# Kernel optimization log

Measured on AMD Instinct MI355X. Metric: run time of the kernel, lower is better.

Reference implementation:

```python
import jax, jax.numpy as jnp
import numpy as np

NUM_HEADS = 32
HEAD_DIM = 128
NUM_KV_HEADS = 8
SCALE = 0.08838834764831845  # 1/sqrt(128)
T = 2048          # total packed tokens (total_q == total_k in delta branch)
N_SAL = 512       # number of salient rows
NUM_SEQS = 4
EPS = 1e-8
NEG = -1e30


def setup_inputs() -> dict:
    key = jax.random.key(0)
    ks = jax.random.split(key, 5)
    q = jax.random.normal(ks[0], (T, NUM_HEADS, HEAD_DIM), dtype=jnp.float32)
    k = jax.random.normal(ks[1], (T, NUM_KV_HEADS, HEAD_DIM), dtype=jnp.float32)
    v = jax.random.normal(ks[2], (N_SAL, NUM_KV_HEADS, HEAD_DIM), dtype=jnp.float32)
    v_cache = jax.random.normal(ks[3], (T, NUM_KV_HEADS, HEAD_DIM), dtype=jnp.float32)
    c_cache = jax.random.normal(ks[4], (T, NUM_HEADS * HEAD_DIM), dtype=jnp.float32)
    # unique, sorted salient row indices (torch index_copy requires well-defined scatter)
    idx_salient_row = (jnp.arange(N_SAL, dtype=jnp.int64) * (T // N_SAL))
    # 4 equal packed sequences
    cu_seqlens = jnp.array([0, 512, 1024, 1536, 2048], dtype=jnp.int64)
    return {"q": q, "k": k, "v": v, "v_cache": v_cache, "c_cache": c_cache,
            "idx_salient_row": idx_salient_row, "cu_seqlens": cu_seqlens}


def _segment_ids(cu_seqlens, n):
    # seg[i] = which packed sequence row i belongs to (searchsorted right on bounds)
    return jnp.searchsorted(cu_seqlens[1:], jnp.arange(n), side="right")


def _sdpa(q_, k_, v_, seg_q_, seg_k_):
    # GQA: repeat_interleave kv heads to match query heads
    n_rep = q_.shape[1] // k_.shape[1]
    if n_rep > 1:
        k_ = jnp.repeat(k_, n_rep, axis=1)
        v_ = jnp.repeat(v_, n_rep, axis=1)
    scores = jnp.einsum("qhd,khd->hqk", q_, k_) * SCALE  # [H, nq, T]
    allow = (seg_q_[:, None] == seg_k_[None, :])          # [nq, T]
    scores = jnp.where(allow[None, :, :], scores, NEG)
    p = jax.nn.softmax(scores, axis=-1)
    return jnp.einsum("hqk,khd->qhd", p, v_)              # [nq, H, D]


def reference(q, k, v, v_cache, c_cache, idx_salient_row, cu_seqlens):
    total = q.shape[0]
    seg = _segment_ids(cu_seqlens, total)  # seg_q == seg_k (total_q == total_k)

    # delta KV-cache update at salient rows
    v_delta = v - v_cache[idx_salient_row]                      # [n_sal, Hkv, D]
    v_delta_sparse = jnp.zeros_like(k).at[idx_salient_row].set(v_delta)
    v_cache_new = v_cache.at[idx_salient_row].set(v)

    # salient-row full attention against updated cache
    o_salient = _sdpa(q[idx_salient_row], k, v_cache_new, seg[idx_salient_row], seg)
    # sparse delta attention for every row
    delta_c = _sdpa(q, k, v_delta_sparse, seg, seg)

    new_c_flat = c_cache + delta_c.reshape(total, -1)
    new_c_flat = new_c_flat.at[idx_salient_row].set(o_salient.reshape(o_salient.shape[0], -1))

    # cosine similarity between old and new context (early-exit signal)
    num = jnp.sum(c_cache * new_c_flat, axis=-1)
    den_c = jnp.sum(c_cache * c_cache, axis=-1)
    den_n = jnp.sum(new_c_flat * new_c_flat, axis=-1)
    cos_sim = num / (jnp.sqrt(den_c) * jnp.sqrt(den_n) + EPS)

    return new_c_flat.reshape(total, NUM_HEADS, HEAD_DIM), cos_sim
```

## Files before the change

### kernel.cpp

```cpp
#include <hip/hip_runtime.h>
#include <math.h>

#define NUM_HEADS 32
#define HEAD_DIM 128
#define NUM_KV_HEADS 8
#define SCALE 0.08838834764831845f
#define EPS 1e-8f
#define MAX_SEG 512
#define QT 32
#define BLK 512
#define SEGC_MAX 16
#define PD_CHUNKS 4
#define SAL_PAD 576
#define PB_STRIDE 520
#define PD_STRIDE 136
#define TLD 130
#define CD (NUM_HEADS * HEAD_DIM)

typedef __bf16 bf16x8 __attribute__((ext_vector_type(8)));
typedef __bf16 bf16x4 __attribute__((ext_vector_type(4)));
typedef float  f32x4  __attribute__((ext_vector_type(4)));

__device__ __forceinline__ int lower_bound_i(const int* __restrict__ a, int n, int key) {
    int lo = 0, hi = n;
    while (lo < hi) { int mid = (lo + hi) >> 1; if (a[mid] < key) lo = mid + 1; else hi = mid; }
    return lo;
}
__device__ __forceinline__ int bsearch_eq(const int* __restrict__ a, int n, int key) {
    int lo = lower_bound_i(a, n, key);
    return (lo < n && a[lo] == key) ? lo : -1;
}

__global__ void prep(const float* __restrict__ k, const float* __restrict__ v,
                     const float* __restrict__ vc, const int* __restrict__ idx,
                     __bf16* __restrict__ kb, __bf16* __restrict__ vnewT,
                     __bf16* __restrict__ vdT, int T, int Tpad, int n_sal,
                     int nb_conv, int nb_vt) {
    __shared__ __bf16 tile[64 * TLD];
    __shared__ int sal_of[64];
    const int b = blockIdx.x;
    const int tid = threadIdx.x;

    if (b < nb_conv) {
        int i = b * 256 + tid;
        int n8 = T * NUM_KV_HEADS * HEAD_DIM / 8;
        if (i < n8) {
            const float4* s4 = (const float4*)(k + (size_t)i * 8);
            float4 a = s4[0], bb = s4[1];
            bf16x8 o;
            o[0]=(__bf16)a.x; o[1]=(__bf16)a.y; o[2]=(__bf16)a.z; o[3]=(__bf16)a.w;
            o[4]=(__bf16)bb.x; o[5]=(__bf16)bb.y; o[6]=(__bf16)bb.z; o[7]=(__bf16)bb.w;
            *(bf16x8*)(kb + (size_t)i * 8) = o;
        }
        return;
    }
    if (b < nb_conv + nb_vt * NUM_KV_HEADS) {
        const int bb = b - nb_conv;
        const int kv = bb / nb_vt;
        const int r0 = (bb % nb_vt) * 64;
        if (tid < 64) sal_of[tid] = bsearch_eq(idx, n_sal, r0 + tid);
        __syncthreads();
        for (int ii = tid; ii < 64 * 32; ii += 256) {
            int r = ii >> 5, c4 = ii & 31;
            int row = r0 + r;
            float4 f = {0.f, 0.f, 0.f, 0.f};
            if (row < T) {
                int s2 = sal_of[r];
                const float* src = (s2 >= 0)
                    ? v  + ((size_t)s2  * NUM_KV_HEADS + kv) * HEAD_DIM
                    : vc + ((size_t)row * NUM_KV_HEADS + kv) * HEAD_DIM;
                f = *(const float4*)(src + c4 * 4);
            }
            __bf16* tp = &tile[r * TLD + c4 * 4];
            tp[0] = (__bf16)f.x; tp[1] = (__bf16)f.y; tp[2] = (__bf16)f.z; tp[3] = (__bf16)f.w;
        }
        __syncthreads();
        for (int ii = tid; ii < 128 * 8; ii += 256) {
            int d = ii >> 3, rg = ii & 7;
            int row_out = r0 + rg * 8;
            if (row_out < Tpad) {
                bf16x8 o;
#pragma unroll
                for (int j = 0; j < 8; j++) o[j] = tile[(rg * 8 + j) * TLD + d];
                *(bf16x8*)(vnewT + ((size_t)kv * HEAD_DIM + d) * Tpad + row_out) = o;
            }
        }
        return;
    }
    {
        const int bb = b - nb_conv - nb_vt * NUM_KV_HEADS;
        const int nvd = SAL_PAD / 64;
        const int kv = bb / nvd;
        const int s0 = (bb % nvd) * 64;
        for (int ii = tid; ii < 64 * 32; ii += 256) {
            int r = ii >> 5, c4 = ii & 31;
            int s = s0 + r;
            float4 f = {0.f, 0.f, 0.f, 0.f};
            if (s < n_sal) {
                int row = idx[s];
                float4 a = *(const float4*)(v  + ((size_t)s   * NUM_KV_HEADS + kv) * HEAD_DIM + c4 * 4);
                float4 bb2 = *(const float4*)(vc + ((size_t)row * NUM_KV_HEADS + kv) * HEAD_DIM + c4 * 4);
                f.x = a.x - bb2.x; f.y = a.y - bb2.y; f.z = a.z - bb2.z; f.w = a.w - bb2.w;
            }
            __bf16* tp = &tile[r * TLD + c4 * 4];
            tp[0] = (__bf16)f.x; tp[1] = (__bf16)f.y; tp[2] = (__bf16)f.z; tp[3] = (__bf16)f.w;
        }
        __syncthreads();
        for (int ii = tid; ii < 128 * 8; ii += 256) {
            int d = ii >> 3, rg = ii & 7;
            bf16x8 o;
#pragma unroll
            for (int j = 0; j < 8; j++) o[j] = tile[(rg * 8 + j) * TLD + d];
            *(bf16x8*)(vdT + ((size_t)kv * HEAD_DIM + d) * SAL_PAD + s0 + rg * 8) = o;
        }
    }
}

__global__ __launch_bounds__(BLK, 4)
void attn_mfma(const float* __restrict__ q, const __bf16* __restrict__ kb,
               const __bf16* __restrict__ vnewT, const __bf16* __restrict__ vdT,
               const float* __restrict__ c_cache, const int* __restrict__ cu,
               const int* __restrict__ idx, float* __restrict__ out_c,
               float* __restrict__ cospart, int T, int Tpad, int n_seq, int n_sal) {
    const int qt    = blockIdx.x;
    const int h     = blockIdx.y;
    const int kvh   = h >> 2;
    const int qrow0 = qt * QT;
    const int tid   = threadIdx.x;
    const int wave  = tid >> 6;
    const int lane  = tid & 63;
    const int lm    = lane & 15;
    const int quad  = lane >> 4;

    __shared__ __align__(16) __bf16 Pb[QT * PB_STRIDE];
    __shared__ __align__(16) __bf16 Pd[QT * PD_STRIDE];
    __shared__ int   scol[MAX_SEG];
    __shared__ float wred[8 * QT];
    __shared__ float linv[QT];
    __shared__ int   salrow[QT];

    int seg_start = 0, seg_end = T;
    for (int s = 0; s < n_seq; s++) {
        int a = cu[s], bnd = cu[s + 1];
        if (qrow0 >= a && qrow0 < bnd) { seg_start = a; seg_end = bnd; }
    }
    const int seg_len = seg_end - seg_start;
    const int s_lo = lower_bound_i(idx, n_sal, seg_start);
    const int s_hi = lower_bound_i(idx, n_sal, seg_end);
    const int nss  = s_hi - s_lo;
    const int ntiles = (seg_len + 15) >> 4;
    const int SEGC   = (seg_len + 31) >> 5;

    const int dim = wave * 16 + lm;

    const float* cbase = c_cache + (size_t)qrow0 * CD + h * HEAD_DIM + dim;
    float cold[2][4];
#pragma unroll
    for (int rt = 0; rt < 2; rt++)
#pragma unroll
        for (int r = 0; r < 4; r++)
            cold[rt][r] = cbase[(size_t)(rt * 16 + quad * 4 + r) * CD];

    if (tid < QT) salrow[tid] = bsearch_eq(idx, n_sal, qrow0 + tid);
    for (int s = tid; s < nss; s += BLK) scol[s] = idx[s_lo + s] - seg_start;
    if (ntiles * 16 < SEGC * 32) {
        for (int ii = tid; ii < QT * 16; ii += BLK) {
            int row = ii >> 4, col = ntiles * 16 + (ii & 15);
            Pb[row * PB_STRIDE + col] = (__bf16)0.f;
        }
    }

    bf16x8 aq[2][4];
#pragma unroll
    for (int rt = 0; rt < 2; rt++) {
        const float* qp = q + ((size_t)(qrow0 + rt * 16 + lm) * NUM_HEADS + h) * HEAD_DIM + quad * 8;
#pragma unroll
        for (int cc = 0; cc < 4; cc++) {
            float4 f0 = *(const float4*)(qp + cc * 32);
            float4 f1 = *(const float4*)(qp + cc * 32 + 4);
            bf16x8 a;
            a[0]=(__bf16)f0.x; a[1]=(__bf16)f0.y; a[2]=(__bf16)f0.z; a[3]=(__bf16)f0.w;
            a[4]=(__bf16)f1.x; a[5]=(__bf16)f1.y; a[6]=(__bf16)f1.z; a[7]=(__bf16)f1.w;
            aq[rt][cc] = a;
        }
    }

    float ps[2] = {0.f, 0.f};
#pragma unroll
    for (int tt = 0; tt < 4; tt++) {
        const int t = wave * 4 + tt;
        if (t < ntiles) {
            int key = seg_start + t * 16 + lm;
            if (key >= seg_start + seg_len) key = seg_start + seg_len - 1;
            const __bf16* kp = kb + ((size_t)key * NUM_KV_HEADS + kvh) * HEAD_DIM + quad * 8;
            bf16x8 bk[4];
#pragma unroll
            for (int cc = 0; cc < 4; cc++) bk[cc] = *(const bf16x8*)(kp + cc * 32);
            f32x4 acc[2] = {{0.f,0.f,0.f,0.f},{0.f,0.f,0.f,0.f}};
#pragma unroll
            for (int cc = 0; cc < 4; cc++) {
                acc[0] = __builtin_amdgcn_mfma_f32_16x16x32_bf16(bk[cc], aq[0][cc], acc[0], 0, 0, 0);
                acc[1] = __builtin_amdgcn_mfma_f32_16x16x32_bf16(bk[cc], aq[1][cc], acc[1], 0, 0, 0);
            }
#pragma unroll
            for (int rt = 0; rt < 2; rt++) {
                bf16x4 pk;
#pragma unroll
                for (int r = 0; r < 4; r++) {
                    const int kl = t * 16 + quad * 4 + r;
                    float e = (kl < seg_len) ? __expf(acc[rt][r] * SCALE) : 0.f;
                    ps[rt] += e;
                    pk[r] = (__bf16)e;
                }
                *(bf16x4*)&Pb[(rt * 16 + lm) * PB_STRIDE + t * 16 + quad * 4] = pk;
            }
        }
    }
#pragma unroll
    for (int m = 16; m <= 32; m <<= 1) {
        ps[0] += __shfl_xor(ps[0], m, 64);
        ps[1] += __shfl_xor(ps[1], m, 64);
    }
    if (quad == 0) {
        wred[wave * QT + lm]      = ps[0];
        wred[wave * QT + 16 + lm] = ps[1];
    }
    __syncthreads();
    if (tid < QT) {
        float s = 0.f;
#pragma unroll
        for (int w = 0; w < 8; w++) s += wred[w * QT + tid];
        linv[tid] = 1.f / s;
    }

    f32x4 acc0a = {0.f,0.f,0.f,0.f}, acc0b = {0.f,0.f,0.f,0.f};
    f32x4 acc1a = {0.f,0.f,0.f,0.f}, acc1b = {0.f,0.f,0.f,0.f};
    const __bf16* vbase = vnewT + ((size_t)kvh * HEAD_DIM + dim) * Tpad + seg_start + quad * 8;
    const __bf16* pb0 = &Pb[lm * PB_STRIDE + quad * 8];
    const __bf16* pb1 = &Pb[(16 + lm) * PB_STRIDE + quad * 8];

#define PV_BODY(cc)  {                                                              \
        bf16x8 a0 = *(const bf16x8*)(pb0 + (cc) * 32);                              \
        bf16x8 a1 = *(const bf16x8*)(pb1 + (cc) * 32);                              \
        bf16x8 bv = *(const bf16x8*)(vbase + (cc) * 32);                            \
        if ((cc) & 1) {                                                             \
            acc0b = __builtin_amdgcn_mfma_f32_16x16x32_bf16(a0, bv, acc0b, 0, 0, 0);\
            acc1b = __builtin_amdgcn_mfma_f32_16x16x32_bf16(a1, bv, acc1b, 0, 0, 0);\
        } else {                                                                    \
            acc0a = __builtin_amdgcn_mfma_f32_16x16x32_bf16(a0, bv, acc0a, 0, 0, 0);\
            acc1a = __builtin_amdgcn_mfma_f32_16x16x32_bf16(a1, bv, acc1a, 0, 0, 0);\
        } }

    if (SEGC == SEGC_MAX) {
#pragma unroll
        for (int cc = 0; cc < SEGC_MAX; cc++) PV_BODY(cc)
    } else {
        for (int cc = 0; cc < SEGC; cc++) PV_BODY(cc)
    }
    f32x4 accF[2];
    accF[0] = acc0a + acc0b;
    accF[1] = acc1a + acc1b;

    f32x4 accD[2] = {{0.f,0.f,0.f,0.f},{0.f,0.f,0.f,0.f}};
    const int ndc = (nss + 31) >> 5;
    const bool al8 = ((s_lo & 7) == 0);
    const __bf16* vdbase = vdT + ((size_t)kvh * HEAD_DIM + dim) * SAL_PAD + s_lo + quad * 8;
    for (int base = 0; base < ndc; base += PD_CHUNKS) {
        const int bc = min(PD_CHUNKS, ndc - base);
        __syncthreads();
        for (int ii = tid; ii < QT * PD_CHUNKS * 32; ii += BLK) {
            int row = ii >> 7, srel = ii & 127;
            int s = base * 32 + srel;
            __bf16 e = (__bf16)0.f;
            if (srel < bc * 32 && s < nss) e = Pb[row * PB_STRIDE + scol[s]];
            Pd[row * PD_STRIDE + srel] = e;
        }
        __syncthreads();
#pragma unroll
        for (int dc = 0; dc < PD_CHUNKS; dc++) {
            if (dc < bc) {
                bf16x8 a0 = *(const bf16x8*)&Pd[lm * PD_STRIDE + dc * 32 + quad * 8];
                bf16x8 a1 = *(const bf16x8*)&Pd[(16 + lm) * PD_STRIDE + dc * 32 + quad * 8];
                const __bf16* vp = vdbase + (base + dc) * 32;
                bf16x8 bv;
                if (al8) bv = *(const bf16x8*)vp;
                else {
#pragma unroll
                    for (int j = 0; j < 8; j++) bv[j] = vp[j];
                }
                accD[0] = __builtin_amdgcn_mfma_f32_16x16x32_bf16(a0, bv, accD[0], 0, 0, 0);
                accD[1] = __builtin_amdgcn_mfma_f32_16x16x32_bf16(a1, bv, accD[1], 0, 0, 0);
            }
        }
    }
    __syncthreads();

    float* cp = (float*)Pd;
    float* obase = out_c + (size_t)qrow0 * CD + h * HEAD_DIM + dim;
#pragma unroll
    for (int rt = 0; rt < 2; rt++) {
#pragma unroll
        for (int r = 0; r < 4; r++) {
            const int row = rt * 16 + quad * 4 + r;
            const float c_old = cold[rt][r];
            const float li = linv[row];
            float o;
            if (salrow[row] >= 0) o = accF[rt][r] * li;
            else                  o = c_old + accD[rt][r] * li;
            obase[(size_t)row * CD] = o;
            float xn = o * c_old, xc = c_old * c_old, xd = o * o;
#pragma unroll
            for (int m = 1; m <= 8; m <<= 1) {
                xn += __shfl_xor(xn, m, 64);
                xc += __shfl_xor(xc, m, 64);
                xd += __shfl_xor(xd, m, 64);
            }
            if (lm == 0) {
                cp[(wave * 3 + 0) * QT + row] = xn;
                cp[(wave * 3 + 1) * QT + row] = xc;
                cp[(wave * 3 + 2) * QT + row] = xd;
            }
        }
    }
    __syncthreads();
    for (int ii = tid; ii < 3 * QT; ii += BLK) {
        int c = ii >> 5, row = ii & 31;
        float s = 0.f;
#pragma unroll
        for (int w = 0; w < 8; w++) s += cp[(w * 3 + c) * QT + row];
        cospart[((size_t)(qrow0 + row) * NUM_HEADS + h) * 3 + c] = s;
    }
}

__global__ void cos_finalize(const float* __restrict__ cospart, float* __restrict__ out_cos, int T) {
    int i = blockIdx.x * blockDim.x + threadIdx.x;
    if (i < T) {
        const float* p = cospart + (size_t)i * NUM_HEADS * 3;
        float n = 0.f, c = 0.f, d = 0.f;
#pragma unroll
        for (int h2 = 0; h2 < NUM_HEADS; h2++) {
            n += p[h2 * 3 + 0]; c += p[h2 * 3 + 1]; d += p[h2 * 3 + 2];
        }
        out_cos[i] = n / (sqrtf(c) * sqrtf(d) + EPS);
    }
}

extern "C" void kernel_launch(void* const* d_in, const int* in_sizes, int n_in,
                              void* d_out, int out_size, void* d_ws, size_t ws_size,
                              hipStream_t stream) {
    const float* q       = (const float*)d_in[0];
    const float* k       = (const float*)d_in[1];
    const float* v       = (const float*)d_in[2];
    const float* v_cache = (const float*)d_in[3];
    const float* c_cache = (const float*)d_in[4];
    const int*   idx     = (const int*)d_in[5];
    const int*   cu      = (const int*)d_in[6];

    const int T     = in_sizes[0] / CD;
    const int n_sal = in_sizes[5];
    const int n_seq = in_sizes[6] - 1;
    const int Tpad  = T + 32;

    float* out_c   = (float*)d_out;
    float* out_cos = out_c + (size_t)T * CD;

    char* wsp = (char*)d_ws;
    size_t off = 0;
    __bf16* kb = (__bf16*)(wsp + off);
    off += (((size_t)T * NUM_KV_HEADS * HEAD_DIM * 2) + 255) & ~(size_t)255;
    __bf16* vnewT = (__bf16*)(wsp + off);
    off += (((size_t)NUM_KV_HEADS * HEAD_DIM * Tpad * 2) + 255) & ~(size_t)255;
    __bf16* vdT = (__bf16*)(wsp + off);
    off += ((size_t)NUM_KV_HEADS * HEAD_DIM * SAL_PAD * 2 + 255) & ~(size_t)255;
    float* cospart = (float*)(wsp + off);
    off += ((size_t)T * NUM_HEADS * 3 * 4 + 255) & ~(size_t)255;
    (void)ws_size;

    const int nb_conv = (T * NUM_KV_HEADS * HEAD_DIM / 8 + 255) / 256;
    const int nb_vt   = (Tpad + 63) / 64;
    const int nb_vd   = SAL_PAD / 64;
    const int nb_tot  = nb_conv + nb_vt * NUM_KV_HEADS + nb_vd * NUM_KV_HEADS;

    prep<<<nb_tot, 256, 0, stream>>>(k, v, v_cache, idx, kb, vnewT, vdT,
                                     T, Tpad, n_sal, nb_conv, nb_vt);

    dim3 grid(T / QT, NUM_HEADS);
    attn_mfma<<<grid, BLK, 0, stream>>>(q, kb, vnewT, vdT, c_cache, cu, idx,
                                        out_c, cospart, T, Tpad, n_seq, n_sal);

    cos_finalize<<<(T + 255) / 256, 256, 0, stream>>>(cospart, out_cos, T);
}
```

Measured before the change: 233.1 us.

## Compute full PV only for salient rows and gather delta P directly from LDS

Only salient query rows, compacted via a ballot, now get the full P·V_new MFMA pass. Non-salient rows skip it and use only the sparse delta product. The delta operand is gathered straight from the Pb shared buffer instead of going through a staging Pd buffer with extra barriers. Per-tile segment bounds and a row-to-salient map are precomputed in an extra prep block, replacing per-block loops and binary searches. Other changes: occupancy hint raised to 8, explicit FULLSEG specialisation of the QK loop, s_setprio around the MFMA section, and a transposed cospart layout with a wave-reduced finalize. The scattered byte gathers from LDS and the extra salient-row passes add complexity and divergence.

```diff
diff --git a/kernel.cpp b/kernel.cpp
--- a/kernel.cpp
+++ b/kernel.cpp
@@ -10,10 +10,8 @@
 #define QT 32
 #define BLK 512
 #define SEGC_MAX 16
-#define PD_CHUNKS 4
 #define SAL_PAD 576
 #define PB_STRIDE 520
-#define PD_STRIDE 136
 #define TLD 130
 #define CD (NUM_HEADS * HEAD_DIM)
 
@@ -31,10 +29,31 @@
     return (lo < n && a[lo] == key) ? lo : -1;
 }
 
+__device__ __forceinline__ bf16x8 cvt8(const float* p) {
+    float4 f0 = *(const float4*)p;
+    float4 f1 = *(const float4*)(p + 4);
+    bf16x8 a;
+    a[0]=(__bf16)f0.x; a[1]=(__bf16)f0.y; a[2]=(__bf16)f0.z; a[3]=(__bf16)f0.w;
+    a[4]=(__bf16)f1.x; a[5]=(__bf16)f1.y; a[6]=(__bf16)f1.z; a[7]=(__bf16)f1.w;
+    return a;
+}
+
+__device__ __forceinline__ void red16(float& xn, float& xc, float& xd) {
+#pragma unroll
+    for (int m = 1; m <= 8; m <<= 1) {
+        xn += __shfl_xor(xn, m, 64);
+        xc += __shfl_xor(xc, m, 64);
+        xd += __shfl_xor(xd, m, 64);
+    }
+}
+
 __global__ void prep(const float* __restrict__ k, const float* __restrict__ v,
                      const float* __restrict__ vc, const int* __restrict__ idx,
+                     const int* __restrict__ cu,
                      __bf16* __restrict__ kb, __bf16* __restrict__ vnewT,
-                     __bf16* __restrict__ vdT, int T, int Tpad, int n_sal,
+                     __bf16* __restrict__ vdT, int* __restrict__ tinfo,
+                     int* __restrict__ rowsal,
+                     int T, int Tpad, int n_sal, int n_seq,
                      int nb_conv, int nb_vt) {
     __shared__ __bf16 tile[64 * TLD];
     __shared__ int sal_of[64];
@@ -87,7 +106,7 @@
         }
         return;
     }
-    {
+    if (b < nb_conv + nb_vt * NUM_KV_HEADS + (SAL_PAD / 64) * NUM_KV_HEADS) {
         const int bb = b - nb_conv - nb_vt * NUM_KV_HEADS;
         const int nvd = SAL_PAD / 64;
         const int kv = bb / nvd;
@@ -113,15 +132,82 @@
             for (int j = 0; j < 8; j++) o[j] = tile[(rg * 8 + j) * TLD + d];
             *(bf16x8*)(vdT + ((size_t)kv * HEAD_DIM + d) * SAL_PAD + s0 + rg * 8) = o;
         }
-    }
-}
-
-__global__ __launch_bounds__(BLK, 4)
+        return;
+    }
+    {
+        for (int i = tid; i < T; i += 256) rowsal[i] = -1;
+        __syncthreads();
+        for (int s = tid; s < n_sal; s += 256) rowsal[idx[s]] = s;
+        const int NT = T / QT;
+        for (int t = tid; t < NT; t += 256) {
+            const int r0 = t * QT;
+            int a = 0, e = T;
+            for (int s = 0; s < n_seq; s++) {
+                int x = cu[s], y = cu[s + 1];
+                if (r0 >= x && r0 < y) { a = x; e = y; }
+            }
+            tinfo[t * 4 + 0] = a;
+            tinfo[t * 4 + 1] = e;
+            tinfo[t * 4 + 2] = lower_bound_i(idx, n_sal, a);
+            tinfo[t * 4 + 3] = lower_bound_i(idx, n_sal, e);
+        }
+    }
+}
+
+
+#define QK_TILE(ttc, FULLSEG) {                                                             \
+    const int t_ = wave * 4 + (ttc);                                                        \
+    if ((FULLSEG) || t_ < ntiles) {                                                         \
+        int key_ = seg_start + t_ * 16 + lm;                                                \
+        if (!(FULLSEG) && key_ >= seg_end) key_ = seg_end - 1;                              \
+        const __bf16* kp_ = kb + ((size_t)key_ * NUM_KV_HEADS + kvh) * HEAD_DIM + quad * 8; \
+        const bf16x8 bk0_ = *(const bf16x8*)(kp_);                                          \
+        const bf16x8 bk1_ = *(const bf16x8*)(kp_ + 32);                                     \
+        const bf16x8 bk2_ = *(const bf16x8*)(kp_ + 64);                                     \
+        const bf16x8 bk3_ = *(const bf16x8*)(kp_ + 96);                                     \
+        f32x4 a0_ = {0.f,0.f,0.f,0.f}, a1_ = {0.f,0.f,0.f,0.f};                             \
+        a0_ = __builtin_amdgcn_mfma_f32_16x16x32_bf16(bk0_, aq00, a0_, 0, 0, 0);            \
+        a1_ = __builtin_amdgcn_mfma_f32_16x16x32_bf16(bk0_, aq10, a1_, 0, 0, 0);            \
+        a0_ = __builtin_amdgcn_mfma_f32_16x16x32_bf16(bk1_, aq01, a0_, 0, 0, 0);            \
+        a1_ = __builtin_amdgcn_mfma_f32_16x16x32_bf16(bk1_, aq11, a1_, 0, 0, 0);            \
+        a0_ = __builtin_amdgcn_mfma_f32_16x16x32_bf16(bk2_, aq02, a0_, 0, 0, 0);            \
+        a1_ = __builtin_amdgcn_mfma_f32_16x16x32_bf16(bk2_, aq12, a1_, 0, 0, 0);            \
+        a0_ = __builtin_amdgcn_mfma_f32_16x16x32_bf16(bk3_, aq03, a0_, 0, 0, 0);            \
+        a1_ = __builtin_amdgcn_mfma_f32_16x16x32_bf16(bk3_, aq13, a1_, 0, 0, 0);            \
+        bf16x4 pk0_, pk1_;                                                                  \
+        _Pragma("unroll")                                                                   \
+        for (int r_ = 0; r_ < 4; r_++) {                                                    \
+            const int kl_ = t_ * 16 + quad * 4 + r_;                                        \
+            const bool ok_ = (FULLSEG) || (kl_ < seg_len);                                  \
+            float e0_ = ok_ ? __expf(a0_[r_] * SCALE) : 0.f;                                \
+            float e1_ = ok_ ? __expf(a1_[r_] * SCALE) : 0.f;                                \
+            ps0 += e0_; ps1 += e1_;                                                         \
+            pk0_[r_] = (__bf16)e0_; pk1_[r_] = (__bf16)e1_;                                 \
+        }                                                                                   \
+        *(bf16x4*)&Pb[lm * PB_STRIDE + t_ * 16 + quad * 4] = pk0_;                          \
+        *(bf16x4*)&Pb[(16 + lm) * PB_STRIDE + t_ * 16 + quad * 4] = pk1_;                   \
+    } }
+
+#define PVG_BODY(cc) {                                                                      \
+    const bf16x8 bv_ = *(const bf16x8*)(vbase + (cc) * 32);                                 \
+    const bf16x8 ax_ = *(const bf16x8*)(pgx + (cc) * 32);                                   \
+    if ((cc) & 1) gO = __builtin_amdgcn_mfma_f32_16x16x32_bf16(ax_, bv_, gO, 0, 0, 0);      \
+    else          gE = __builtin_amdgcn_mfma_f32_16x16x32_bf16(ax_, bv_, gE, 0, 0, 0); }
+
+#define PVG_LOOP()                                                                          \
+    if (SEGC == SEGC_MAX) {                                                                 \
+        _Pragma("unroll")                                                                   \
+        for (int cc = 0; cc < SEGC_MAX; cc++) PVG_BODY(cc)                                  \
+    } else {                                                                                \
+        for (int cc = 0; cc < SEGC; cc++) PVG_BODY(cc)                                      \
+    }
+
+__global__ __launch_bounds__(BLK, 8)
 void attn_mfma(const float* __restrict__ q, const __bf16* __restrict__ kb,
                const __bf16* __restrict__ vnewT, const __bf16* __restrict__ vdT,
-               const float* __restrict__ c_cache, const int* __restrict__ cu,
-               const int* __restrict__ idx, float* __restrict__ out_c,
-               float* __restrict__ cospart, int T, int Tpad, int n_seq, int n_sal) {
+               const float* __restrict__ c_cache, const int* __restrict__ tinfo,
+               const int* __restrict__ rowsal, const int* __restrict__ idx,
+               float* __restrict__ out_c, float* __restrict__ cospart, int Tpad) {
     const int qt    = blockIdx.x;
     const int h     = blockIdx.y;
     const int kvh   = h >> 2;
@@ -133,36 +219,32 @@
     const int quad  = lane >> 4;
 
     __shared__ __align__(16) __bf16 Pb[QT * PB_STRIDE];
-    __shared__ __align__(16) __bf16 Pd[QT * PD_STRIDE];
-    __shared__ int   scol[MAX_SEG];
+    __shared__ int   scolb[MAX_SEG];
     __shared__ float wred[8 * QT];
     __shared__ float linv[QT];
     __shared__ int   salrow[QT];
-
-    int seg_start = 0, seg_end = T;
-    for (int s = 0; s < n_seq; s++) {
-        int a = cu[s], bnd = cu[s + 1];
-        if (qrow0 >= a && qrow0 < bnd) { seg_start = a; seg_end = bnd; }
-    }
+    __shared__ int   growS[QT];
+    __shared__ int   ngS;
+    __shared__ float cp[8 * 3 * QT];
+
+    const int4 ti = *(const int4*)(tinfo + qt * 4);
+    const int seg_start = ti.x, seg_end = ti.y, s_lo = ti.z, s_hi = ti.w;
     const int seg_len = seg_end - seg_start;
-    const int s_lo = lower_bound_i(idx, n_sal, seg_start);
-    const int s_hi = lower_bound_i(idx, n_sal, seg_end);
-    const int nss  = s_hi - s_lo;
+    const int nss    = s_hi - s_lo;
     const int ntiles = (seg_len + 15) >> 4;
     const int SEGC   = (seg_len + 31) >> 5;
-
     const int dim = wave * 16 + lm;
 
-    const float* cbase = c_cache + (size_t)qrow0 * CD + h * HEAD_DIM + dim;
-    float cold[2][4];
-#pragma unroll
-    for (int rt = 0; rt < 2; rt++)
-#pragma unroll
-        for (int r = 0; r < 4; r++)
-            cold[rt][r] = cbase[(size_t)(rt * 16 + quad * 4 + r) * CD];
-
-    if (tid < QT) salrow[tid] = bsearch_eq(idx, n_sal, qrow0 + tid);
-    for (int s = tid; s < nss; s += BLK) scol[s] = idx[s_lo + s] - seg_start;
+    int sr_reg = -1;
+    if (tid < QT) { sr_reg = rowsal[qrow0 + tid]; salrow[tid] = sr_reg; }
+    if (tid < 64) {
+        bool p = (tid < QT) && (sr_reg >= 0);
+        unsigned long long mk = __ballot(p);
+        if (tid < QT) growS[tid] = 0;
+        if (p) growS[__popcll(mk & ((1ull << tid) - 1ull))] = tid;
+        if (tid == 0) ngS = (int)__popcll(mk);
+    }
+    for (int s = tid; s < nss; s += BLK) scolb[s] = (idx[s_lo + s] - seg_start) * 2;
     if (ntiles * 16 < SEGC * 32) {
         for (int ii = tid; ii < QT * 16; ii += BLK) {
             int row = ii >> 4, col = ntiles * 16 + (ii & 15);
@@ -170,60 +252,28 @@
         }
     }
 
-    bf16x8 aq[2][4];
-#pragma unroll
-    for (int rt = 0; rt < 2; rt++) {
-        const float* qp = q + ((size_t)(qrow0 + rt * 16 + lm) * NUM_HEADS + h) * HEAD_DIM + quad * 8;
-#pragma unroll
-        for (int cc = 0; cc < 4; cc++) {
-            float4 f0 = *(const float4*)(qp + cc * 32);
-            float4 f1 = *(const float4*)(qp + cc * 32 + 4);
-            bf16x8 a;
-            a[0]=(__bf16)f0.x; a[1]=(__bf16)f0.y; a[2]=(__bf16)f0.z; a[3]=(__bf16)f0.w;
-            a[4]=(__bf16)f1.x; a[5]=(__bf16)f1.y; a[6]=(__bf16)f1.z; a[7]=(__bf16)f1.w;
-            aq[rt][cc] = a;
-        }
-    }
-
-    float ps[2] = {0.f, 0.f};
-#pragma unroll
-    for (int tt = 0; tt < 4; tt++) {
-        const int t = wave * 4 + tt;
-        if (t < ntiles) {
-            int key = seg_start + t * 16 + lm;
-            if (key >= seg_start + seg_len) key = seg_start + seg_len - 1;
-            const __bf16* kp = kb + ((size_t)key * NUM_KV_HEADS + kvh) * HEAD_DIM + quad * 8;
-            bf16x8 bk[4];
-#pragma unroll
-            for (int cc = 0; cc < 4; cc++) bk[cc] = *(const bf16x8*)(kp + cc * 32);
-            f32x4 acc[2] = {{0.f,0.f,0.f,0.f},{0.f,0.f,0.f,0.f}};
-#pragma unroll
-            for (int cc = 0; cc < 4; cc++) {
-                acc[0] = __builtin_amdgcn_mfma_f32_16x16x32_bf16(bk[cc], aq[0][cc], acc[0], 0, 0, 0);
-                acc[1] = __builtin_amdgcn_mfma_f32_16x16x32_bf16(bk[cc], aq[1][cc], acc[1], 0, 0, 0);
-            }
-#pragma unroll
-            for (int rt = 0; rt < 2; rt++) {
-                bf16x4 pk;
-#pragma unroll
-                for (int r = 0; r < 4; r++) {
-                    const int kl = t * 16 + quad * 4 + r;
-                    float e = (kl < seg_len) ? __expf(acc[rt][r] * SCALE) : 0.f;
-                    ps[rt] += e;
-                    pk[r] = (__bf16)e;
-                }
-                *(bf16x4*)&Pb[(rt * 16 + lm) * PB_STRIDE + t * 16 + quad * 4] = pk;
-            }
-        }
+    bf16x8 aq00, aq01, aq02, aq03, aq10, aq11, aq12, aq13;
+    {
+        const float* qp0 = q + ((size_t)(qrow0 + lm) * NUM_HEADS + h) * HEAD_DIM + quad * 8;
+        const float* qp1 = q + ((size_t)(qrow0 + 16 + lm) * NUM_HEADS + h) * HEAD_DIM + quad * 8;
+        aq00 = cvt8(qp0);      aq01 = cvt8(qp0 + 32); aq02 = cvt8(qp0 + 64); aq03 = cvt8(qp0 + 96);
+        aq10 = cvt8(qp1);      aq11 = cvt8(qp1 + 32); aq12 = cvt8(qp1 + 64); aq13 = cvt8(qp1 + 96);
+    }
+
+    float ps0 = 0.f, ps1 = 0.f;
+    if (seg_len == MAX_SEG) {
+        QK_TILE(0, 1) QK_TILE(1, 1) QK_TILE(2, 1) QK_TILE(3, 1)
+    } else {
+        QK_TILE(0, 0) QK_TILE(1, 0) QK_TILE(2, 0) QK_TILE(3, 0)
     }
 #pragma unroll
     for (int m = 16; m <= 32; m <<= 1) {
-        ps[0] += __shfl_xor(ps[0], m, 64);
-        ps[1] += __shfl_xor(ps[1], m, 64);
+        ps0 += __shfl_xor(ps0, m, 64);
+        ps1 += __shfl_xor(ps1, m, 64);
     }
     if (quad == 0) {
-        wred[wave * QT + lm]      = ps[0];
-        wred[wave * QT + 16 + lm] = ps[1];
+        wred[wave * QT + lm]      = ps0;
+        wred[wave * QT + 16 + lm] = ps1;
     }
     __syncthreads();
     if (tid < QT) {
@@ -233,69 +283,66 @@
         linv[tid] = 1.f / s;
     }
 
-    f32x4 acc0a = {0.f,0.f,0.f,0.f}, acc0b = {0.f,0.f,0.f,0.f};
-    f32x4 acc1a = {0.f,0.f,0.f,0.f}, acc1b = {0.f,0.f,0.f,0.f};
-    const __bf16* vbase = vnewT + ((size_t)kvh * HEAD_DIM + dim) * Tpad + seg_start + quad * 8;
-    const __bf16* pb0 = &Pb[lm * PB_STRIDE + quad * 8];
-    const __bf16* pb1 = &Pb[(16 + lm) * PB_STRIDE + quad * 8];
-
-#define PV_BODY(cc)  {                                                              \
-        bf16x8 a0 = *(const bf16x8*)(pb0 + (cc) * 32);                              \
-        bf16x8 a1 = *(const bf16x8*)(pb1 + (cc) * 32);                              \
-        bf16x8 bv = *(const bf16x8*)(vbase + (cc) * 32);                            \
-        if ((cc) & 1) {                                                             \
-            acc0b = __builtin_amdgcn_mfma_f32_16x16x32_bf16(a0, bv, acc0b, 0, 0, 0);\
-            acc1b = __builtin_amdgcn_mfma_f32_16x16x32_bf16(a1, bv, acc1b, 0, 0, 0);\
-        } else {                                                                    \
-            acc0a = __builtin_amdgcn_mfma_f32_16x16x32_bf16(a0, bv, acc0a, 0, 0, 0);\
-            acc1a = __builtin_amdgcn_mfma_f32_16x16x32_bf16(a1, bv, acc1a, 0, 0, 0);\
-        } }
-
-    if (SEGC == SEGC_MAX) {
-#pragma unroll
-        for (int cc = 0; cc < SEGC_MAX; cc++) PV_BODY(cc)
-    } else {
-        for (int cc = 0; cc < SEGC; cc++) PV_BODY(cc)
-    }
-    f32x4 accF[2];
-    accF[0] = acc0a + acc0b;
-    accF[1] = acc1a + acc1b;
-
-    f32x4 accD[2] = {{0.f,0.f,0.f,0.f},{0.f,0.f,0.f,0.f}};
+    const int ng = ngS;
+
+    const float* cbase = c_cache + (size_t)qrow0 * CD + h * HEAD_DIM + dim;
+    float cold[2][4];
+#pragma unroll
+    for (int rt = 0; rt < 2; rt++)
+#pragma unroll
+        for (int r = 0; r < 4; r++)
+            cold[rt][r] = cbase[(size_t)(rt * 16 + quad * 4 + r) * CD];
+    int crow0[4]; float cg0[4];
+#pragma unroll
+    for (int r = 0; r < 4; r++) { crow0[r] = 0; cg0[r] = 0.f; }
+    if (ng > 0) {
+#pragma unroll
+        for (int r = 0; r < 4; r++) {
+            crow0[r] = growS[quad * 4 + r];
+            cg0[r] = cbase[(size_t)crow0[r] * CD];
+        }
+    }
+
+    __builtin_amdgcn_s_setprio(1);
+    f32x4 accDa = {0.f,0.f,0.f,0.f}, accDb = {0.f,0.f,0.f,0.f};
     const int ndc = (nss + 31) >> 5;
     const bool al8 = ((s_lo & 7) == 0);
     const __bf16* vdbase = vdT + ((size_t)kvh * HEAD_DIM + dim) * SAL_PAD + s_lo + quad * 8;
-    for (int base = 0; base < ndc; base += PD_CHUNKS) {
-        const int bc = min(PD_CHUNKS, ndc - base);
-        __syncthreads();
-        for (int ii = tid; ii < QT * PD_CHUNKS * 32; ii += BLK) {
-            int row = ii >> 7, srel = ii & 127;
-            int s = base * 32 + srel;
-            __bf16 e = (__bf16)0.f;
-            if (srel < bc * 32 && s < nss) e = Pb[row * PB_STRIDE + scol[s]];
-            Pd[row * PD_STRIDE + srel] = e;
-        }
-        __syncthreads();
-#pragma unroll
-        for (int dc = 0; dc < PD_CHUNKS; dc++) {
-            if (dc < bc) {
-                bf16x8 a0 = *(const bf16x8*)&Pd[lm * PD_STRIDE + dc * 32 + quad * 8];
-                bf16x8 a1 = *(const bf16x8*)&Pd[(16 + lm) * PD_STRIDE + dc * 32 + quad * 8];
-                const __bf16* vp = vdbase + (base + dc) * 32;
-                bf16x8 bv;
-                if (al8) bv = *(const bf16x8*)vp;
-                else {
-#pragma unroll
-                    for (int j = 0; j < 8; j++) bv[j] = vp[j];
-                }
-                accD[0] = __builtin_amdgcn_mfma_f32_16x16x32_bf16(a0, bv, accD[0], 0, 0, 0);
-                accD[1] = __builtin_amdgcn_mfma_f32_16x16x32_bf16(a1, bv, accD[1], 0, 0, 0);
-            }
-        }
-    }
+    const char* pbrow0 = (const char*)&Pb[lm * PB_STRIDE];
+    const char* pbrow1 = (const char*)&Pb[(16 + lm) * PB_STRIDE];
+    for (int dc = 0; dc < ndc; dc++) {
+        bf16x8 bvD;
+        const __bf16* vp = vdbase + dc * 32;
+        if (al8) bvD = *(const bf16x8*)vp;
+        else {
+#pragma unroll
+            for (int j = 0; j < 8; j++) bvD[j] = vp[j];
+        }
+        bf16x8 aD0, aD1;
+#pragma unroll
+        for (int j = 0; j < 8; j++) {
+            int s = dc * 32 + quad * 8 + j;
+            int cb = (s < nss) ? scolb[s] : -1;
+            __bf16 e0 = (__bf16)0.f, e1 = (__bf16)0.f;
+            if (cb >= 0) {
+                e0 = *(const __bf16*)(pbrow0 + cb);
+                e1 = *(const __bf16*)(pbrow1 + cb);
+            }
+            aD0[j] = e0; aD1[j] = e1;
+        }
+        accDa = __builtin_amdgcn_mfma_f32_16x16x32_bf16(aD0, bvD, accDa, 0, 0, 0);
+        accDb = __builtin_amdgcn_mfma_f32_16x16x32_bf16(aD1, bvD, accDb, 0, 0, 0);
+    }
+
+    const __bf16* vbase = vnewT + ((size_t)kvh * HEAD_DIM + dim) * Tpad + seg_start + quad * 8;
+    f32x4 gE = {0.f,0.f,0.f,0.f}, gO = {0.f,0.f,0.f,0.f};
+    if (ng > 0) {
+        const __bf16* pgx = &Pb[growS[lm] * PB_STRIDE + quad * 8];
+        PVG_LOOP()
+    }
+    __builtin_amdgcn_s_setprio(0);
     __syncthreads();
 
-    float* cp = (float*)Pd;
     float* obase = out_c + (size_t)qrow0 * CD + h * HEAD_DIM + dim;
 #pragma unroll
     for (int rt = 0; rt < 2; rt++) {
@@ -303,22 +350,57 @@
         for (int r = 0; r < 4; r++) {
             const int row = rt * 16 + quad * 4 + r;
             const float c_old = cold[rt][r];
-            const float li = linv[row];
-            float o;
-            if (salrow[row] >= 0) o = accF[rt][r] * li;
-            else                  o = c_old + accD[rt][r] * li;
-            obase[(size_t)row * CD] = o;
+            const float aD = (rt == 0) ? accDa[r] : accDb[r];
+            const bool ns = (salrow[row] < 0);
+            const float o = c_old + aD * linv[row];
+            if (ns) obase[(size_t)row * CD] = o;
             float xn = o * c_old, xc = c_old * c_old, xd = o * o;
-#pragma unroll
-            for (int m = 1; m <= 8; m <<= 1) {
-                xn += __shfl_xor(xn, m, 64);
-                xc += __shfl_xor(xc, m, 64);
-                xd += __shfl_xor(xd, m, 64);
-            }
-            if (lm == 0) {
+            red16(xn, xc, xd);
+            if (lm == 0 && ns) {
                 cp[(wave * 3 + 0) * QT + row] = xn;
                 cp[(wave * 3 + 1) * QT + row] = xc;
                 cp[(wave * 3 + 2) * QT + row] = xd;
+            }
+        }
+    }
+    if (ng > 0) {
+        f32x4 accG = gE + gO;
+#pragma unroll
+        for (int r = 0; r < 4; r++) {
+            const int slot = quad * 4 + r;
+            const int crow = crow0[r];
+            const float co = cg0[r];
+            const float o = accG[r] * linv[crow];
+            const bool act = (slot < ng);
+            if (act) obase[(size_t)crow * CD] = o;
+            float xn = o * co, xc = co * co, xd = o * o;
+            red16(xn, xc, xd);
+            if (lm == 0 && act) {
+                cp[(wave * 3 + 0) * QT + crow] = xn;
+                cp[(wave * 3 + 1) * QT + crow] = xc;
+                cp[(wave * 3 + 2) * QT + crow] = xd;
+            }
+        }
+        if (ng > 16) {
+            const __bf16* pgx = &Pb[growS[16 + lm] * PB_STRIDE + quad * 8];
+            gE = (f32x4){0.f,0.f,0.f,0.f}; gO = (f32x4){0.f,0.f,0.f,0.f};
+            PVG_LOOP()
+            f32x4 accG1 = gE + gO;
+#pragma unroll
+            for (int r = 0; r < 4; r++) {
+                const int slot = 16 + quad * 4 + r;
+                const int crow = growS[slot];
+                const float co = cbase[(size_t)crow * CD];
+                const float o = accG1[r] * linv[crow];
+                const bool act = (slot < ng);
+                if (act) obase[(size_t)crow * CD] = o;
+                float xn = o * co, xc = co * co, xd = o * o;
+                red16(xn, xc, xd);
+                if (lm == 0 && act) {
+                    cp[(wave * 3 + 0) * QT + crow] = xn;
+                    cp[(wave * 3 + 1) * QT + crow] = xc;
+                    cp[(wave * 3 + 2) * QT + crow] = xd;
+                }
             }
         }
     }
@@ -328,21 +410,24 @@
         float s = 0.f;
 #pragma unroll
         for (int w = 0; w < 8; w++) s += cp[(w * 3 + c) * QT + row];
-        cospart[((size_t)(qrow0 + row) * NUM_HEADS + h) * 3 + c] = s;
+        cospart[((size_t)(qrow0 + row) * 3 + c) * NUM_HEADS + h] = s;
     }
 }
 
 __global__ void cos_finalize(const float* __restrict__ cospart, float* __restrict__ out_cos, int T) {
-    int i = blockIdx.x * blockDim.x + threadIdx.x;
-    if (i < T) {
-        const float* p = cospart + (size_t)i * NUM_HEADS * 3;
-        float n = 0.f, c = 0.f, d = 0.f;
-#pragma unroll
-        for (int h2 = 0; h2 < NUM_HEADS; h2++) {
-            n += p[h2 * 3 + 0]; c += p[h2 * 3 + 1]; d += p[h2 * 3 + 2];
-        }
-        out_cos[i] = n / (sqrtf(c) * sqrtf(d) + EPS);
-    }
+    const int lane = threadIdx.x & 63;
+    const int row  = blockIdx.x * 4 + (threadIdx.x >> 6);
+    if (row >= T) return;
+    const float* p = cospart + (size_t)row * (NUM_HEADS * 3);
+    float a = p[lane];
+    float b = (lane < 32) ? p[64 + lane] : 0.f;
+#pragma unroll
+    for (int m = 1; m <= 16; m <<= 1) {
+        a += __shfl_xor(a, m, 64);
+        b += __shfl_xor(b, m, 64);
+    }
+    float den_c = __shfl(a, 32, 64);
+    if (lane == 0) out_cos[row] = a / (sqrtf(den_c) * sqrtf(b) + EPS);
 }
 
 extern "C" void kernel_launch(void* const* d_in, const int* in_sizes, int n_in,
@@ -360,6 +445,7 @@
     const int n_sal = in_sizes[5];
     const int n_seq = in_sizes[6] - 1;
     const int Tpad  = T + 32;
+    const int NT    = T / QT;
 
     float* out_c   = (float*)d_out;
     float* out_cos = out_c + (size_t)T * CD;
@@ -374,19 +460,24 @@
     off += ((size_t)NUM_KV_HEADS * HEAD_DIM * SAL_PAD * 2 + 255) & ~(size_t)255;
     float* cospart = (float*)(wsp + off);
     off += ((size_t)T * NUM_HEADS * 3 * 4 + 255) & ~(size_t)255;
+    int* tinfo = (int*)(wsp + off);
+    off += ((size_t)NT * 4 * 4 + 255) & ~(size_t)255;
+    int* rowsal = (int*)(wsp + off);
+    off += ((size_t)T * 4 + 255) & ~(size_t)255;
     (void)ws_size;
 
     const int nb_conv = (T * NUM_KV_HEADS * HEAD_DIM / 8 + 255) / 256;
     const int nb_vt   = (Tpad + 63) / 64;
     const int nb_vd   = SAL_PAD / 64;
-    const int nb_tot  = nb_conv + nb_vt * NUM_KV_HEADS + nb_vd * NUM_KV_HEADS;
-
-    prep<<<nb_tot, 256, 0, stream>>>(k, v, v_cache, idx, kb, vnewT, vdT,
-                                     T, Tpad, n_sal, nb_conv, nb_vt);
+    const int nb_tot  = nb_conv + nb_vt * NUM_KV_HEADS + nb_vd * NUM_KV_HEADS + 1;
+
+    prep<<<nb_tot, 256, 0, stream>>>(k, v, v_cache, idx, cu, kb, vnewT, vdT,
+                                     tinfo, rowsal, T, Tpad, n_sal, n_seq,
+                                     nb_conv, nb_vt);
 
     dim3 grid(T / QT, NUM_HEADS);
-    attn_mfma<<<grid, BLK, 0, stream>>>(q, kb, vnewT, vdT, c_cache, cu, idx,
-                                        out_c, cospart, T, Tpad, n_seq, n_sal);
-
-    cos_finalize<<<(T + 255) / 256, 256, 0, stream>>>(cospart, out_cos, T);
-}
+    attn_mfma<<<grid, BLK, 0, stream>>>(q, kb, vnewT, vdT, c_cache, tinfo, rowsal,
+                                        idx, out_c, cospart, Tpad);
+
+    cos_finalize<<<(T + 3) / 4, 256, 0, stream>>>(cospart, out_cos, T);
+}
```

After: 267.6 us. +14.8%, slower.
